# Performance work log

Measured on AMD Instinct MI355X. Metric: run time of the kernel, lower is better.

## Reference

```python
import jax, jax.numpy as jnp
import numpy as np

B, N, K = 8, 1024, 9
T = B * N
EPS_BN = 1e-5


def _knn_idx(x, k):
    # x: [n, d] -> [n, k] indices of k nearest neighbours (self included, dist 0)
    x = jax.lax.stop_gradient(x)
    sq = jnp.sum(x * x, axis=1)
    d = sq[:, None] + sq[None, :] - 2.0 * (x @ x.T)
    return jax.lax.top_k(-d, k)[1]


def _mlp_bn(x, params):
    # PyG MLP with plain_last=True: linear->BN->ReLU for all but last layer, last is linear.
    n = len(params)
    for i, (W, b, g, be) in enumerate(params):
        x = x @ W + b
        if i < n - 1:
            mu = jnp.mean(x, axis=0)
            var = jnp.var(x, axis=0)  # biased, as torch BN (training stats)
            x = g * (x - mu) * jax.lax.rsqrt(var + EPS_BN) + be
            x = jax.nn.relu(x)
    return x


def _edge_conv(x, idx, params):
    # DynamicEdgeConv: message = MLP([x_i, x_j - x_i]), aggr='mean' over k neighbours
    n, k = idx.shape
    xj = x[idx]                                   # [n,k,c] gather
    xi = jnp.broadcast_to(x[:, None, :], xj.shape)
    e = jnp.concatenate([xi, xj - xi], axis=-1).reshape(n * k, -1)
    h = _mlp_bn(e, params)                        # [n*k, c_out]
    return h.reshape(n, k, -1).mean(axis=1)       # mean aggregation


def _dgcnn(x, c1, c3, head, lin2_W, lin2_b):
    # conv1: kNN within each graph (batch-aware)
    xb = x.reshape(B, N, -1)
    idx = jax.vmap(lambda g: _knn_idx(g, K))(xb)                 # [B,N,K] local
    idx = (idx + (jnp.arange(B) * N)[:, None, None]).reshape(T, K)
    x1 = _edge_conv(x, idx, c1)                                  # [T,128]
    # head MLP (norm=None, dropout inactive in eval)
    h = x1
    for i, (W, b) in enumerate(head):
        h = h @ W + b
        if i < len(head) - 1:
            h = jax.nn.relu(h)
    out = (h - jnp.mean(h)) / (jnp.std(h, ddof=1) + 1e-5)        # torch.std unbiased
    out = jax.nn.sigmoid(out)                                    # [T,1] gate
    xl = out * x
    xs = (1.0 - out) * x
    # conv3 called without batch -> global kNN over all T nodes
    xl = _edge_conv(xl, _knn_idx(xl, K), c3)                     # [T,16]
    xs = _edge_conv(xs, _knn_idx(xs, K), c3)
    xl = xl.reshape(B, N, -1).max(axis=1)                        # global_max_pool
    xs = xs.reshape(B, N, -1).max(axis=1)
    mass = jnp.concatenate([xl, xs], axis=1) @ lin2_W + lin2_b   # [B,1]
    return mass.flatten()


_PARAM_SHAPES = {
    'c1_W1': (8, 128), 'c1_b1': (128,), 'c1_g1': (128,), 'c1_be1': (128,),
    'c1_W2': (128, 128), 'c1_b2': (128,), 'c1_g2': (128,), 'c1_be2': (128,),
    'c1_W3': (128, 128), 'c1_b3': (128,),
    'c3_W1': (8, 64), 'c3_b1': (64,), 'c3_g1': (64,), 'c3_be1': (64,),
    'c3_W2': (64, 64), 'c3_b2': (64,), 'c3_g2': (64,), 'c3_be2': (64,),
    'c3_W3': (64, 16), 'c3_b3': (16,),
    'h_W1': (128, 64), 'h_b1': (64,),
    'h_W2': (64, 32), 'h_b2': (32,),
    'h_W3': (32, 1), 'h_b3': (1,),
    'lin2_W': (32, 1), 'lin2_b': (1,),
}


def setup_inputs() -> dict:
    key = jax.random.key(0)
    ks = jax.random.split(key, len(_PARAM_SHAPES) + 1)
    inp = {'x': jax.random.normal(ks[0], (T, 4), dtype=jnp.float32)}
    for i, (name, shp) in enumerate(_PARAM_SHAPES.items()):
        v = jax.random.normal(ks[i + 1], shp, dtype=jnp.float32) * 0.1
        if '_g' in name:
            v = v + 1.0
        inp[name] = v
    return inp


def reference(x, c1_W1, c1_b1, c1_g1, c1_be1, c1_W2, c1_b2, c1_g2, c1_be2,
              c1_W3, c1_b3, c3_W1, c3_b1, c3_g1, c3_be1, c3_W2, c3_b2, c3_g2,
              c3_be2, c3_W3, c3_b3, h_W1, h_b1, h_W2, h_b2, h_W3, h_b3,
              lin2_W, lin2_b):
    c1 = [(c1_W1, c1_b1, c1_g1, c1_be1), (c1_W2, c1_b2, c1_g2, c1_be2),
          (c1_W3, c1_b3, None, None)]
    c3 = [(c3_W1, c3_b1, c3_g1, c3_be1), (c3_W2, c3_b2, c3_g2, c3_be2),
          (c3_W3, c3_b3, None, None)]
    head = [(h_W1, h_b1), (h_W2, h_b2), (h_W3, h_b3)]
    return _dgcnn(x, c1, c3, head, lin2_W, lin2_b)
```

## Files before the change

### kernel.cpp

```cpp
#include <hip/hip_runtime.h>
#include <math.h>

#define TN 8192
#define KNN 9
#define NPG 1024
#define TK (TN*KNN)
#define CPCL 12
#define NCHG 32
#define CPCG 16

__device__ __forceinline__ float sqnorm(float4 v){
  return fmaf(v.x,v.x,fmaf(v.y,v.y,fmaf(v.z,v.z,v.w*v.w)));
}
__device__ __forceinline__ float pairdist(float4 a, float sqa, float4 b, float sqb){
  float dot = fmaf(a.x,b.x,fmaf(a.y,b.y,fmaf(a.z,b.z,a.w*b.w)));
  return sqa + sqb - 2.0f*dot;
}
__device__ __forceinline__ void chain9(float (&bd)[9], float d){
  float t=d;
  #pragma unroll
  for(int p=0;p<9;p++){
    float lo=fminf(bd[p],t);
    t=fmaxf(bd[p],t);
    bd[p]=lo;
// ... 394 lines not shown

__global__ void k_bn2q(const double* __restrict__ Md, const float* __restrict__ W2,
      const float* __restrict__ g, const float* __restrict__ be,
      float* __restrict__ scale, float* __restrict__ shift){
  __shared__ double redq[128], redt[128];
  __shared__ float sw[128];
  int c = blockIdx.x, t = threadIdx.x;
  sw[t] = W2[t*128+c];
  __syncthreads();
  double zb = Md[16384+t]/(double)TK;
  double inner=0;
  for(int j=0;j<128;j++) inner += Md[t*128+j]*(double)sw[j];
  redq[t] = (double)sw[t]*(inner/(double)TK);
  redt[t] = (double)sw[t]*zb;
  __syncthreads();
  for(int s=64;s>0;s>>=1){
    if(t<s){ redq[t]+=redq[t+s]; redt[t]+=redt[t+s]; }
    __syncthreads();
  }
  if(t==0){
    double var = redq[0] - redt[0]*redt[0];
    if(var<0) var=0;
    double sc = (double)g[c]/sqrt(var+1e-5);
    scale[c]=(float)sc;
    shift[c]=(float)((double)be[c] - redt[0]*sc);
  }
}

__global__ __launch_bounds__(256) void k_midagg(const float4* __restrict__ x,
      const int* __restrict__ idx, const float* __restrict__ W1,
      const float* __restrict__ sc1, const float* __restrict__ sh1,
      const float* __restrict__ W2, const float* __restrict__ sc2,
      const float* __restrict__ sh2, float* __restrict__ Zb){
  __shared__ float sa[72][9];
  __shared__ float sW1[8*128];
  __shared__ float sZ[72*132];
  const int tid = threadIdx.x;
  const int node0 = blockIdx.x*8;
  if(tid<256) ((float4*)sW1)[tid] = ((const float4*)W1)[tid];
  if(tid<72){
    int e = blockIdx.x*72 + tid;
    int i = e/KNN; int j = idx[e];
    float4 xi = x[i], xj = x[j];
    sa[tid][0]=xi.x; sa[tid][1]=xi.y; sa[tid][2]=xi.z; sa[tid][3]=xi.w;
    sa[tid][4]=xj.x-xi.x; sa[tid][5]=xj.y-xi.y; sa[tid][6]=xj.z-xi.z; sa[tid][7]=xj.w-xi.w;
  }
  __syncthreads();
  for(int f=tid; f<2304; f+=256){
    int e = f>>5, c4 = f&31;
    float4 scv = ((const float4*)sc1)[c4];
    float4 shv = ((const float4*)sh1)[c4];
    float4 y = make_float4(0.f,0.f,0.f,0.f);
    #pragma unroll
    for(int k=0;k<8;k++){
      float a = sa[e][k];
      float4 wv = *(const float4*)(sW1 + k*128 + c4*4);
      y.x=fmaf(a,wv.x,y.x); y.y=fmaf(a,wv.y,y.y);
      y.z=fmaf(a,wv.z,y.z); y.w=fmaf(a,wv.w,y.w);
    }
    float4 z;
    z.x = fmaxf(fmaf(scv.x,y.x,shv.x),0.f);
    z.y = fmaxf(fmaf(scv.y,y.y,shv.y),0.f);
    z.z = fmaxf(fmaf(scv.z,y.z,shv.z),0.f);
    z.w = fmaxf(fmaf(scv.w,y.w,shv.w),0.f);
    *(float4*)(sZ + e*132 + c4*4) = z;
  }
  __syncthreads();
  const int tc = tid & 31, tr = tid >> 5;
  float acc[9][4];
  #pragma unroll
  for(int s=0;s<9;s++)
    #pragma unroll
    for(int e=0;e<4;e++) acc[s][e]=0.f;
  #pragma unroll 2
  for(int k4=0;k4<32;k4++){
    float4 av[9];
    #pragma unroll
    for(int s=0;s<9;s++) av[s] = *(const float4*)(sZ + (tr*9+s)*132 + k4*4);
    #pragma unroll
    for(int kk=0;kk<4;kk++){
      float4 bv = *(const float4*)(W2 + (size_t)(k4*4+kk)*128 + tc*4);
      #pragma unroll
      for(int s=0;s<9;s++){
        float a = (kk==0)?av[s].x:(kk==1)?av[s].y:(kk==2)?av[s].z:av[s].w;
        acc[s][0]=fmaf(a,bv.x,acc[s][0]);
        acc[s][1]=fmaf(a,bv.y,acc[s][1]);
        acc[s][2]=fmaf(a,bv.z,acc[s][2]);
        acc[s][3]=fmaf(a,bv.w,acc[s][3]);
      }
    }
  }
  float4 scv = ((const float4*)sc2)[tc];
  float4 shv = ((const float4*)sh2)[tc];
  float4 sum = make_float4(0.f,0.f,0.f,0.f);
  #pragma unroll
  for(int s=0;s<9;s++){
    sum.x += fmaxf(fmaf(scv.x,acc[s][0],shv.x),0.f);
    sum.y += fmaxf(fmaf(scv.y,acc[s][1],shv.y),0.f);
    sum.z += fmaxf(fmaf(scv.z,acc[s][2],shv.z),0.f);
    sum.w += fmaxf(fmaf(scv.w,acc[s][3],shv.w),0.f);
  }
  sum.x*=(1.f/9.f); sum.y*=(1.f/9.f); sum.z*=(1.f/9.f); sum.w*=(1.f/9.f);
  *(float4*)(Zb + (size_t)(node0+tr)*128 + tc*4) = sum;
}

__global__ __launch_bounds__(256) void k_gemm128(const float* __restrict__ A,
      const float* __restrict__ W, const float* __restrict__ bias,
      float* __restrict__ out){
  __shared__ float sZ[64*132];
  const int tid = threadIdx.x;
  const int row0 = blockIdx.x*64;
  for(int e=tid; e<64*32; e+=256){
    int r = e>>5, c4 = e&31;
    ((float4*)(sZ + r*132))[c4] = ((const float4*)(A + (size_t)(row0+r)*128))[c4];
  }
  __syncthreads();
  const int tc = tid & 31, tr = tid >> 5;
  float acc[8][4];
  #pragma unroll
  for(int rr=0;rr<8;rr++)
    #pragma unroll
    for(int e=0;e<4;e++) acc[rr][e]=0.f;
  #pragma unroll 4
  for(int k4=0;k4<32;k4++){
    float4 av[8];
    #pragma unroll
    for(int rr=0;rr<8;rr++) av[rr] = *(const float4*)(sZ + (tr+rr*8)*132 + k4*4);
    #pragma unroll
    for(int kk=0;kk<4;kk++){
      float4 bv = *(const float4*)(W + (size_t)(k4*4+kk)*128 + tc*4);
      #pragma unroll
      for(int rr=0;rr<8;rr++){
        float a = (kk==0)?av[rr].x:(kk==1)?av[rr].y:(kk==2)?av[rr].z:av[rr].w;
        acc[rr][0]=fmaf(a,bv.x,acc[rr][0]);
        acc[rr][1]=fmaf(a,bv.y,acc[rr][1]);
        acc[rr][2]=fmaf(a,bv.z,acc[rr][2]);
        acc[rr][3]=fmaf(a,bv.w,acc[rr][3]);
      }
    }
  }
  float4 breg = *(const float4*)(bias + tc*4);
  #pragma unroll
  for(int rr=0;rr<8;rr++){
    int r = row0 + tr + rr*8;
    float4 vals;
    vals.x = acc[rr][0]+breg.x;
    vals.y = acc[rr][1]+breg.y;
    vals.z = acc[rr][2]+breg.z;
    vals.w = acc[rr][3]+breg.w;
    *(float4*)(out + (size_t)r*128 + tc*4) = vals;
  }
}

__global__ __launch_bounds__(256) void k_l1d(const float4* __restrict__ xa,
        const float4* __restrict__ xb, const int* __restrict__ ia,
        const int* __restrict__ ib, const float* __restrict__ W,
        const float* __restrict__ bias, float* __restrict__ Ybase,
        float* __restrict__ pstat){
  constexpr int NOUT = 64;
  __shared__ float sA[64][9];
  __shared__ float sW[8*NOUT];
  __shared__ float ssum[NOUT], ssq2[NOUT];
  const int by = blockIdx.y;
  const float4* x = by ? xb : xa;
  const int* idx = by ? ib : ia;
  float* Y = Ybase + (size_t)by*TK*NOUT;
  const int tid = threadIdx.x;
  const int row0 = blockIdx.x*64;
  if(tid < 64){
    int r = row0 + tid;
    int i = r/KNN;
    int j = idx[r];
    float4 xi = x[i], xj = x[j];
    sA[tid][0]=xi.x; sA[tid][1]=xi.y; sA[tid][2]=xi.z; sA[tid][3]=xi.w;
    sA[tid][4]=xj.x-xi.x; sA[tid][5]=xj.y-xi.y; sA[tid][6]=xj.z-xi.z; sA[tid][7]=xj.w-xi.w;
  }
  for(int e=tid; e<8*NOUT/4; e+=256) ((float4*)sW)[e] = ((const float4*)W)[e];
  if(tid < NOUT){ ssum[tid]=0.f; ssq2[tid]=0.f; }
  __syncthreads();
  const int tc = tid & 15, tr = tid >> 4;
  float acc[4][4];
  #pragma unroll
  for(int rr=0;rr<4;rr++)
    #pragma unroll
    for(int cc=0;cc<4;cc++) acc[rr][cc]=0.f;
  #pragma unroll
  for(int k=0;k<8;k++){
    float a[4];
    #pragma unroll
    for(int rr=0;rr<4;rr++) a[rr]=sA[tr*4+rr][k];
    #pragma unroll
    for(int cc=0;cc<4;cc++){
      float bv = sW[k*NOUT + tc*4 + cc];
      #pragma unroll
      for(int rr=0;rr<4;rr++) acc[rr][cc]=fmaf(a[rr],bv,acc[rr][cc]);
    }
  }
  float breg[4];
  #pragma unroll
  for(int cc=0;cc<4;cc++) breg[cc]=bias[tc*4+cc];
  float ls[4], lq[4];
  #pragma unroll
  for(int cc=0;cc<4;cc++){ls[cc]=0.f;lq[cc]=0.f;}
  #pragma unroll
  for(int rr=0;rr<4;rr++){
    int r = row0 + tr*4 + rr;
    float vals[4];
    #pragma unroll
    for(int u=0;u<4;u++){
      float val = acc[rr][u] + breg[u];
      vals[u]=val; ls[u]+=val; lq[u]+=val*val;
    }
    *(float4*)(Y + (size_t)r*NOUT + tc*4) = make_float4(vals[0],vals[1],vals[2],vals[3]);
  }
  #pragma unroll
  for(int cc=0;cc<4;cc++){
    atomicAdd(&ssum[tc*4+cc], ls[cc]);
    atomicAdd(&ssq2[tc*4+cc], lq[cc]);
  }
  __syncthreads();
  if(tid < NOUT){
    size_t pb = ((size_t)by*1152 + blockIdx.x)*2*NOUT;
    pstat[pb + tid] = ssum[tid];
    pstat[pb + NOUT + tid] = ssq2[tid];
  }
}

__global__ __launch_bounds__(256) void k_psum(const float* __restrict__ pstat,
      double* __restrict__ pp, int nblk, int twoC){
  size_t base = (size_t)blockIdx.y*nblk*twoC;
  int per = (nblk+7)/8;
  int b0 = blockIdx.x*per;
  int b1 = b0+per; if(b1>nblk) b1=nblk;
  for(int e=threadIdx.x; e<twoC; e+=256){
    double s=0;
    for(int b=b0;b<b1;b++) s += (double)pstat[base + (size_t)b*twoC + e];
    pp[((size_t)blockIdx.y*8 + blockIdx.x)*twoC + e] = s;
  }
}

__global__ void k_finalized(const double* __restrict__ pp,
     const float* __restrict__ g, const float* __restrict__ be,
     float* __restrict__ scale, float* __restrict__ shift, double M){
  int prob = threadIdx.x >> 6, c = threadIdx.x & 63;
  double S=0,Q=0;
  for(int b=0;b<8;b++){
    S+=pp[((size_t)prob*8+b)*128 + c];
    Q+=pp[((size_t)prob*8+b)*128 + 64 + c];
  }
  double mu = S/M;
  double var = Q/M - mu*mu;
  if(var < 0) var = 0;
  double sc = (double)g[c] / sqrt(var + 1e-5);
  scale[prob*64+c] = (float)sc;
  shift[prob*64+c] = (float)((double)be[c] - mu*sc);
}

__global__ __launch_bounds__(512,4) void k_mid64d(float* __restrict__ Ybase,
        const float* __restrict__ W, const float* __restrict__ bias,
        const float* __restrict__ scale2, const float* __restrict__ shift2,
        float* __restrict__ pstat){
  constexpr int C = 64;
  constexpr int CPAD = 68;
  __shared__ float sZ[128*CPAD];
  __shared__ float sW[64*C];
  __shared__ float ssum[C], ssq2[C];
  const int by = blockIdx.y;
  float* Y = Ybase + (size_t)by*TK*C;
  const float* scale = scale2 + by*C;
  const float* shift = shift2 + by*C;
  const int tid = threadIdx.x;
  const int row0 = blockIdx.x*128;
  for(int e=tid; e<128*16; e+=512){
    int r = e>>4, c4 = e&15;
    float4 v = ((const float4*)(Y + (size_t)(row0+r)*C))[c4];
    float4 sc = ((const float4*)scale)[c4];
    float4 sh = ((const float4*)shift)[c4];
    v.x = fmaxf(fmaf(sc.x,v.x,sh.x), 0.f);
    v.y = fmaxf(fmaf(sc.y,v.y,sh.y), 0.f);
    v.z = fmaxf(fmaf(sc.z,v.z,sh.z), 0.f);
    v.w = fmaxf(fmaf(sc.w,v.w,sh.w), 0.f);
    ((float4*)(sZ + r*CPAD))[c4] = v;
  }
  for(int e=tid; e<64*C/4; e+=512) ((float4*)sW)[e] = ((const float4*)W)[e];
  if(tid < C){ ssum[tid]=0.f; ssq2[tid]=0.f; }
  __syncthreads();
  const int tc = tid & 15, tr = tid >> 4;
  float acc[4][4];
  #pragma unroll
  for(int rr=0;rr<4;rr++)
    #pragma unroll
    for(int e=0;e<4;e++) acc[rr][e]=0.f;
  #pragma unroll 4
  for(int k4=0;k4<16;k4++){
    float4 av[4];
    #pragma unroll
    for(int rr=0;rr<4;rr++) av[rr] = *(const float4*)(sZ + (tr+rr*32)*CPAD + k4*4);
    #pragma unroll
    for(int kk=0;kk<4;kk++){
      float4 bv = *(const float4*)(sW + (k4*4+kk)*C + tc*4);
      #pragma unroll
      for(int rr=0;rr<4;rr++){
        float a = (kk==0)?av[rr].x:(kk==1)?av[rr].y:(kk==2)?av[rr].z:av[rr].w;
        acc[rr][0]=fmaf(a,bv.x,acc[rr][0]);
        acc[rr][1]=fmaf(a,bv.y,acc[rr][1]);
        acc[rr][2]=fmaf(a,bv.z,acc[rr][2]);
        acc[rr][3]=fmaf(a,bv.w,acc[rr][3]);
      }
    }
  }
  float4 breg = *(const float4*)(bias + tc*4);
  float ls[4]={0,0,0,0}, lq[4]={0,0,0,0};
  #pragma unroll
  for(int rr=0;rr<4;rr++){
    int r = row0 + tr + rr*32;
    float4 vals;
    vals.x = acc[rr][0]+breg.x;
    vals.y = acc[rr][1]+breg.y;
    vals.z = acc[rr][2]+breg.z;
    vals.w = acc[rr][3]+breg.w;
    ls[0]+=vals.x; lq[0]+=vals.x*vals.x;
    ls[1]+=vals.y; lq[1]+=vals.y*vals.y;
    ls[2]+=vals.z; lq[2]+=vals.z*vals.z;
    ls[3]+=vals.w; lq[3]+=vals.w*vals.w;
    *(float4*)(Y + (size_t)r*C + tc*4) = vals;
  }
  #pragma unroll
  for(int e=0;e<4;e++){
    atomicAdd(&ssum[tc*4+e], ls[e]);
    atomicAdd(&ssq2[tc*4+e], lq[e]);
  }
  __syncthreads();
  if(tid < C){
    size_t pb = ((size_t)by*576 + blockIdx.x)*2*C;
    pstat[pb + tid] = ssum[tid];
    pstat[pb + C + tid] = ssq2[tid];
  }
}

__global__ __launch_bounds__(256) void k_agg_gemmd(const float* __restrict__ Ybase,
      const float* __restrict__ scale2, const float* __restrict__ shift2,
      const float* __restrict__ W, const float* __restrict__ bias,
      float* __restrict__ outl, float* __restrict__ outs){
  constexpr int KIN=64, NOUT=16;
  constexpr int CPAD = KIN+4;
  __shared__ float sZ[64*CPAD];
  __shared__ float sW[KIN*NOUT];
  const int by = blockIdx.y;
  const float* Y = Ybase + (size_t)by*TK*KIN;
  const float* scale = scale2 + by*KIN;
  const float* shift = shift2 + by*KIN;
  float* out = by ? outs : outl;
  const int tid = threadIdx.x;
  const int node0 = blockIdx.x*64;
  for(int e=tid; e<64*KIN/4; e+=256){
    int r = e/(KIN/4), c4 = e%(KIN/4);
    float4 sc = ((const float4*)scale)[c4];
    float4 sh = ((const float4*)shift)[c4];
    const float4* src = (const float4*)(Y + (size_t)(node0+r)*KNN*KIN) + c4;
    float4 s = make_float4(0.f,0.f,0.f,0.f);
    #pragma unroll
    for(int j=0;j<KNN;j++){
      float4 v = src[(size_t)j*(KIN/4)];
      s.x += fmaxf(fmaf(sc.x,v.x,sh.x),0.f);
      s.y += fmaxf(fmaf(sc.y,v.y,sh.y),0.f);
      s.z += fmaxf(fmaf(sc.z,v.z,sh.z),0.f);
      s.w += fmaxf(fmaf(sc.w,v.w,sh.w),0.f);
    }
    s.x*=(1.f/9.f); s.y*=(1.f/9.f); s.z*=(1.f/9.f); s.w*=(1.f/9.f);
    ((float4*)(sZ + r*CPAD))[c4] = s;
  }
  for(int e=tid; e<KIN*NOUT/4; e+=256) ((float4*)sW)[e] = ((const float4*)W)[e];
  __syncthreads();
  const int tc = tid & 15, tr = tid >> 4;
  float acc[4] = {0.f,0.f,0.f,0.f};
  for(int k4=0;k4<KIN/4;k4++){
    float4 av[4];
    #pragma unroll
    for(int rr=0;rr<4;rr++) av[rr] = *(const float4*)(sZ + (tr+rr*16)*CPAD + k4*4);
    #pragma unroll
    for(int kk=0;kk<4;kk++){
      float bv = sW[(k4*4+kk)*NOUT + tc];
      #pragma unroll
      for(int rr=0;rr<4;rr++){
        float a = (kk==0)?av[rr].x:(kk==1)?av[rr].y:(kk==2)?av[rr].z:av[rr].w;
        acc[rr]=fmaf(a,bv,acc[rr]);
      }
    }
  }
  #pragma unroll
  for(int rr=0;rr<4;rr++){
    int r = node0 + tr + rr*16;
    out[(size_t)r*NOUT + tc] = acc[rr] + bias[tc];
  }
}

__global__ __launch_bounds__(256) void k_head(const float* __restrict__ x1,
    const float* __restrict__ W1, const float* __restrict__ b1,
    const float* __restrict__ W2, const float* __restrict__ b2,
    const float* __restrict__ W3, const float* __restrict__ b3,
    float* __restrict__ h, float* __restrict__ pstat){
  __shared__ float sA[32*132];
  __shared__ float sW1[128*64];
  __shared__ float o1[32*68];
  __shared__ float sW2[64*32];
  __shared__ float o2[32*33];
  __shared__ float sb1[64], sb2[32], sW3v[32];
  __shared__ float rs[32], rq[32];
  const int tid = threadIdx.x;
  const int row0 = blockIdx.x*32;
  for(int e=tid; e<32*32; e+=256){
    int r = e>>5, c4 = e&31;
    ((float4*)(sA + r*132))[c4] = ((const float4*)(x1 + (size_t)(row0+r)*128))[c4];
  }
  for(int e=tid; e<128*64/4; e+=256) ((float4*)sW1)[e] = ((const float4*)W1)[e];
  for(int e=tid; e<64*32/4; e+=256)  ((float4*)sW2)[e] = ((const float4*)W2)[e];
  if(tid < 64) sb1[tid]=b1[tid];
  if(tid < 32){ sb2[tid]=b2[tid]; sW3v[tid]=W3[tid]; }
  __syncthreads();
  const int tc = tid & 15, tr = tid >> 4;
  float a1[2][4];
  #pragma unroll
  for(int rr=0;rr<2;rr++)
    #pragma unroll
    for(int e=0;e<4;e++) a1[rr][e]=0.f;
  for(int k4=0;k4<32;k4++){
    float4 av0 = *(const float4*)(sA + (tr*2  )*132 + k4*4);
    float4 av1 = *(const float4*)(sA + (tr*2+1)*132 + k4*4);
    #pragma unroll
    for(int kk=0;kk<4;kk++){
      float4 bv = *(const float4*)(sW1 + (k4*4+kk)*64 + tc*4);
      float p0 = (kk==0)?av0.x:(kk==1)?av0.y:(kk==2)?av0.z:av0.w;
      float p1 = (kk==0)?av1.x:(kk==1)?av1.y:(kk==2)?av1.z:av1.w;
      a1[0][0]=fmaf(p0,bv.x,a1[0][0]); a1[0][1]=fmaf(p0,bv.y,a1[0][1]);
      a1[0][2]=fmaf(p0,bv.z,a1[0][2]); a1[0][3]=fmaf(p0,bv.w,a1[0][3]);
      a1[1][0]=fmaf(p1,bv.x,a1[1][0]); a1[1][1]=fmaf(p1,bv.y,a1[1][1]);
      a1[1][2]=fmaf(p1,bv.z,a1[1][2]); a1[1][3]=fmaf(p1,bv.w,a1[1][3]);
    }
  }
  #pragma unroll
  for(int rr=0;rr<2;rr++)
    #pragma unroll
    for(int e=0;e<4;e++)
      o1[(tr*2+rr)*68 + tc*4+e] = fmaxf(a1[rr][e]+sb1[tc*4+e], 0.f);
  __syncthreads();
  float a2[2][2] = {{0.f,0.f},{0.f,0.f}};
  for(int k=0;k<64;k++){
    float w0 = sW2[k*32 + tc*2], w1 = sW2[k*32 + tc*2+1];
    float v0 = o1[(tr*2  )*68 + k];
    float v1 = o1[(tr*2+1)*68 + k];
    a2[0][0]=fmaf(v0,w0,a2[0][0]); a2[0][1]=fmaf(v0,w1,a2[0][1]);
    a2[1][0]=fmaf(v1,w0,a2[1][0]); a2[1][1]=fmaf(v1,w1,a2[1][1]);
  }
  #pragma unroll
  for(int rr=0;rr<2;rr++)
    #pragma unroll
    for(int cc=0;cc<2;cc++)
      o2[(tr*2+rr)*33 + tc*2+cc] = fmaxf(a2[rr][cc]+sb2[tc*2+cc], 0.f);
  __syncthreads();
  if(tid < 32){
    float hv = b3[0];
    #pragma unroll
    for(int k=0;k<32;k++) hv = fmaf(o2[tid*33+k], sW3v[k], hv);
    h[row0+tid]=hv;
    rs[tid]=hv; rq[tid]=hv*hv;
  }
  __syncthreads();
  if(tid==0){
    float S=0.f, Q=0.f;
    #pragma unroll
    for(int i=0;i<32;i++){ S+=rs[i]; Q+=rq[i]; }
    pstat[blockIdx.x*2]=S; pstat[blockIdx.x*2+1]=Q;
  }
}

__global__ __launch_bounds__(256) void k_fin_h(const float* __restrict__ pstat,
      float* __restrict__ hpar){
  __shared__ double sS[256], sQ[256];
  int t = threadIdx.x;
  sS[t] = (double)pstat[2*t]; sQ[t] = (double)pstat[2*t+1];
  __syncthreads();
  for(int s=128;s>0;s>>=1){
    if(t<s){ sS[t]+=sS[t+s]; sQ[t]+=sQ[t+s]; }
    __syncthreads();
  }
  if(t==0){
    double mu = sS[0]/8192.0;
    double var = (sQ[0] - 8192.0*mu*mu)/8191.0;
    double sd = (var > 0) ? sqrt(var) : 0.0;
    hpar[0]=(float)mu;
    hpar[1]=(float)(1.0/(sd + 1e-5));
  }
}

__global__ __launch_bounds__(256) void k_gate(const float* __restrict__ h,
      const float* __restrict__ hpar, const float4* __restrict__ x,
      float4* __restrict__ xl, float4* __restrict__ xs){
  int i = blockIdx.x*256 + threadIdx.x;
  float z = (h[i]-hpar[0])*hpar[1];
  float o = 1.0f/(1.0f+expf(-z));
  float om = 1.0f - o;
  float4 v = x[i];
  xl[i] = make_float4(o*v.x, o*v.y, o*v.z, o*v.w);
  xs[i] = make_float4(om*v.x, om*v.y, om*v.z, om*v.w);
}

__global__ __launch_bounds__(256) void k_final(const float* __restrict__ xlf,
      const float* __restrict__ xsf, const float* __restrict__ W,
      const float* __restrict__ b, float* __restrict__ out){
  __shared__ float red[32][8];
  int g = blockIdx.x;
  int c = threadIdx.x & 31;
  int chunk = threadIdx.x >> 5;
  const float* src = (c < 16) ? xlf : xsf;
  int ch = (c < 16) ? c : c-16;
  float m = -1e30f;
  for(int n=chunk*128; n<chunk*128+128; n++)
    m = fmaxf(m, src[((size_t)g*1024+n)*16 + ch]);
  red[c][chunk]=m;
  __syncthreads();
  if(threadIdx.x < 32){
    float mm = red[threadIdx.x][0];
    #pragma unroll
    for(int p=1;p<8;p++) mm = fmaxf(mm, red[threadIdx.x][p]);
    red[threadIdx.x][0]=mm;
  }
  __syncthreads();
  if(threadIdx.x == 0){
    float acc = b[0];
    for(int cc=0;cc<32;cc++) acc = fmaf(red[cc][0], W[cc], acc);
    out[g]=acc;
  }
}

extern "C" void kernel_launch(void* const* d_in, const int* in_sizes, int n_in,
                              void* d_out, int out_size, void* d_ws, size_t ws_size,
                              hipStream_t stream){
  const float* x    =(const float*)d_in[0];
  const float* c1W1 =(const float*)d_in[1];
  const float* c1g1 =(const float*)d_in[3];
  const float* c1be1=(const float*)d_in[4];
  const float* c1W2 =(const float*)d_in[5];
  const float* c1g2 =(const float*)d_in[7];
  const float* c1be2=(const float*)d_in[8];
  const float* c1W3 =(const float*)d_in[9];
  const float* c1b3 =(const float*)d_in[10];
  const float* c3W1 =(const float*)d_in[11];
  const float* c3b1 =(const float*)d_in[12];
  const float* c3g1 =(const float*)d_in[13];
  const float* c3be1=(const float*)d_in[14];
  const float* c3W2 =(const float*)d_in[15];
  const float* c3b2 =(const float*)d_in[16];
  const float* c3g2 =(const float*)d_in[17];
  const float* c3be2=(const float*)d_in[18];
  const float* c3W3 =(const float*)d_in[19];
  const float* c3b3 =(const float*)d_in[20];
  const float* hW1  =(const float*)d_in[21];
  const float* hb1  =(const float*)d_in[22];
  const float* hW2  =(const float*)d_in[23];
  const float* hb2  =(const float*)d_in[24];
  const float* hW3  =(const float*)d_in[25];
  const float* hb3  =(const float*)d_in[26];
  const float* l2W  =(const float*)d_in[27];
  const float* l2b  =(const float*)d_in[28];
  (void)in_sizes; (void)n_in; (void)out_size; (void)ws_size;

  char* wsb=(char*)d_ws;
  size_t off=0;
  auto alloc=[&](size_t bytes)->char*{
    char* p = wsb + off;
    off = (off + bytes + 255) & ~(size_t)255;
    return p;
  };
  float* Y    =(float*)alloc((size_t)TK*128*4);
  float* x1   =(float*)alloc((size_t)TN*128*4);
  float* Zb   =(float*)alloc((size_t)TN*128*4);
  int*   idx1 =(int*)  alloc((size_t)TK*4);
  int*   idxl =(int*)  alloc((size_t)TK*4);
  int*   idxs =(int*)  alloc((size_t)TK*4);
  float* pd   =(float*)alloc((size_t)2*TN*72*4);
  float* h    =(float*)alloc((size_t)TN*4);
  float* xl   =(float*)alloc((size_t)TN*16);
  float* xs   =(float*)alloc((size_t)TN*16);
  float* xlf  =(float*)alloc((size_t)TN*16*4);
  float* xsf  =(float*)alloc((size_t)TN*16*4);
  float* pstat=(float*)alloc((size_t)2304*128*4);
  double* pp  =(double*)alloc((size_t)16*256*8);
  double* Md  =(double*)alloc((size_t)16512*8);
  float* mp44 =(float*)alloc((size_t)288*44*4);
  float* tl   =(float*)alloc((size_t)TN*4);
  float* tg   =(float*)alloc((size_t)2*TN*4);
  unsigned char* cnt8l=(unsigned char*)alloc((size_t)TN*8);
  unsigned char* cnt8g=(unsigned char*)alloc((size_t)2*TN*NCHG);
  float* bnp  =(float*)alloc(1024*4);
  float* hpar =(float*)alloc(64);

  float* sc1=bnp,      *sh1=bnp+128, *sc2=bnp+256, *sh2=bnp+384;
  float* scA=bnp+512,  *shA=bnp+640, *scB=bnp+768, *shB=bnp+896;
  unsigned short* listl=(unsigned short*)Y;
  unsigned short* listg=(unsigned short*)Y;
  float* mpartM = Y;

  k_part_local  <<<256,256,0,stream>>>((const float4*)x, pd);
  k_thresh_local<<<32, 256,0,stream>>>(pd, tl);
  k_collect_local<<<256,256,0,stream>>>((const float4*)x, tl, cnt8l, listl);
  k_refine_local<<<TN/32,256,0,stream>>>((const float4*)x, cnt8l, listl, idx1);
  k_mom8<<<288,256,0,stream>>>((const float4*)x, idx1, mp44);
  k_bn1q<<<1,128,0,stream>>>(mp44, c1W1, c1g1, c1be1, sc1, sh1);
  k_syrk128<<<288,256,0,stream>>>((const float4*)x, idx1, c1W1, sc1, sh1, mpartM);
  k_redM<<<65,256,0,stream>>>(mpartM, Md);
  k_bn2q<<<128,128,0,stream>>>(Md, c1W2, c1g2, c1be2, sc2, sh2);
  k_midagg<<<1024,256,0,stream>>>((const float4*)x, idx1, c1W1, sc1, sh1, c1W2, sc2, sh2, Zb);
  k_gemm128<<<TN/64,256,0,stream>>>(Zb, c1W3, c1b3, x1);
  k_head<<<TN/32,256,0,stream>>>(x1,hW1,hb1,hW2,hb2,hW3,hb3,h,pstat);
  k_fin_h<<<1,256,0,stream>>>(pstat,hpar);
  k_gate<<<32,256,0,stream>>>(h,hpar,(const float4*)x,(float4*)xl,(float4*)xs);
  k_part_sub   <<<dim3(256,2),256,0,stream>>>((const float4*)xl,(const float4*)xs,pd);
  k_thresh_sub <<<64,256,0,stream>>>(pd,tg);
  k_collect_glob<<<dim3(512,2),256,0,stream>>>((const float4*)xl,(const float4*)xs,tg,cnt8g,listg);
  k_refine_glob<<<2*TN/32,256,0,stream>>>((const float4*)xl,(const float4*)xs,cnt8g,listg,idxl,idxs);
  k_l1d<<<dim3(1152,2),256,0,stream>>>((const float4*)xl,(const float4*)xs,idxl,idxs,c3W1,c3b1,Y,pstat);
  k_psum<<<dim3(8,2),256,0,stream>>>(pstat, pp, 1152, 128);
  k_finalized<<<1,128,0,stream>>>(pp,c3g1,c3be1,scA,shA,(double)TK);
  k_mid64d<<<dim3(576,2),512,0,stream>>>(Y, c3W2, c3b2, scA, shA, pstat);
  k_psum<<<dim3(8,2),256,0,stream>>>(pstat, pp, 576, 128);
  k_finalized<<<1,128,0,stream>>>(pp,c3g2,c3be2,scB,shB,(double)TK);
  k_agg_gemmd<<<dim3(TN/64,2),256,0,stream>>>(Y, scB, shB, c3W3, c3b3, xlf, xsf);
  k_final<<<8,256,0,stream>>>(xlf,xsf,l2W,l2b,(float*)d_out);
}
```

Baseline: 497.9 us.

## Compute conv3 BatchNorm stats via input moments and Gram matrix, fuse mean-aggregation

The conv3 edge-MLP no longer writes the [TK,64] layer-1 and layer-2 activations to global memory. BN1 statistics now come from first and second moments of the 8-wide edge features projected through W1. BN2 statistics come from a 64x64 Gram matrix of the post-BN1 activations, accumulated per block and reduced in double precision. A fused kernel then recomputes layer1, layer2, BN, ReLU and the mean over the 9 neighbours in shared memory, applying W3 after aggregation. This trades heavy global memory traffic for recomputation and a syrk pass, and relies on the biases cancelling under BN.

```diff
diff --git a/kernel.cpp b/kernel.cpp
--- a/kernel.cpp
+++ b/kernel.cpp
@@ -570,235 +570,289 @@
   }
 }
 
-__global__ __launch_bounds__(256) void k_l1d(const float4* __restrict__ xa,
-        const float4* __restrict__ xb, const int* __restrict__ ia,
-        const int* __restrict__ ib, const float* __restrict__ W,
-        const float* __restrict__ bias, float* __restrict__ Ybase,
-        float* __restrict__ pstat){
-  constexpr int NOUT = 64;
-  __shared__ float sA[64][9];
-  __shared__ float sW[8*NOUT];
-  __shared__ float ssum[NOUT], ssq2[NOUT];
-  const int by = blockIdx.y;
-  const float4* x = by ? xb : xa;
-  const int* idx = by ? ib : ia;
-  float* Y = Ybase + (size_t)by*TK*NOUT;
+__global__ __launch_bounds__(256) void k_mom8d(const float4* __restrict__ xa,
+      const float4* __restrict__ xb, const int* __restrict__ ia,
+      const int* __restrict__ ib, float* __restrict__ mpart){
+  __shared__ float sa[256][9];
+  const int prob = blockIdx.y;
+  const float4* x = prob ? xb : xa;
+  const int* idx = prob ? ib : ia;
+  int t = threadIdx.x;
+  int e = blockIdx.x*256 + t;
+  int i = e/KNN; int j = idx[e];
+  float4 xi = x[i], xj = x[j];
+  sa[t][0]=xi.x; sa[t][1]=xi.y; sa[t][2]=xi.z; sa[t][3]=xi.w;
+  sa[t][4]=xj.x-xi.x; sa[t][5]=xj.y-xi.y; sa[t][6]=xj.z-xi.z; sa[t][7]=xj.w-xi.w;
+  __syncthreads();
+  if(t < 44){
+    float s=0.f;
+    if(t<8){
+      for(int e2=0;e2<256;e2++) s += sa[e2][t];
+    } else {
+      int f=t-8, p=0, q=0, acc=0;
+      for(p=0;p<8;p++){ int cnt=8-p; if(f<acc+cnt){ q=p+(f-acc); break;} acc+=cnt; }
+      for(int e2=0;e2<256;e2++) s += sa[e2][p]*sa[e2][q];
+    }
+    mpart[((size_t)prob*288 + blockIdx.x)*44 + t]=s;
+  }
+}
+
+__global__ void k_bn1qd(const float* __restrict__ mpart, const float* __restrict__ W1,
+      const float* __restrict__ g, const float* __restrict__ be,
+      float* __restrict__ scale, float* __restrict__ shift){
+  __shared__ double mom[2][44];
+  int t = threadIdx.x;
+  if(t<88){
+    int pr=t/44, m=t%44;
+    double s=0; for(int b=0;b<288;b++) s+=(double)mpart[((size_t)pr*288+b)*44+m];
+    mom[pr][m]=s;
+  }
+  __syncthreads();
+  int prob = t>>6, c = t&63;
+  double m[8], w[8];
+  #pragma unroll
+  for(int p=0;p<8;p++){ m[p]=mom[prob][p]/(double)TK; w[p]=(double)W1[p*64+c]; }
+  double q=0.0; int f=8;
+  for(int p=0;p<8;p++)
+    for(int qq=p;qq<8;qq++){
+      double cov = mom[prob][f]/(double)TK - m[p]*m[qq];
+      q += (p==qq?1.0:2.0)*w[p]*w[qq]*cov;
+      f++;
+    }
+  if(q<0) q=0;
+  double sc = (double)g[c]/sqrt(q+1e-5);
+  double mu=0; for(int p=0;p<8;p++) mu += m[p]*w[p];
+  scale[prob*64+c]=(float)sc;
+  shift[prob*64+c]=(float)((double)be[c] - mu*sc);
+}
+
+__global__ __launch_bounds__(256) void k_syrk64d(const float4* __restrict__ xa,
+      const float4* __restrict__ xb, const int* __restrict__ ia,
+      const int* __restrict__ ib, const float* __restrict__ W1,
+      const float* __restrict__ sc0, const float* __restrict__ sh0,
+      float* __restrict__ mpartM){
+  __shared__ float sa[64][9];
+  __shared__ float sW1[8*64];
+  __shared__ float sZ[64*68];
+  __shared__ float ssum[64];
+  const int prob = blockIdx.y;
+  const float4* x = prob ? xb : xa;
+  const int* idx = prob ? ib : ia;
+  const float* sc1 = sc0 + prob*64;
+  const float* sh1 = sh0 + prob*64;
+  const int tid = threadIdx.x;
+  if(tid<128) ((float4*)sW1)[tid] = ((const float4*)W1)[tid];
+  if(tid<64) ssum[tid]=0.f;
+  const int zc4 = tid & 15, ze0 = tid >> 4;
+  const int i0 = (tid>>4)*4, j0 = (tid&15)*4;
+  float acc[4][4];
+  #pragma unroll
+  for(int a=0;a<4;a++)
+    #pragma unroll
+    for(int b=0;b<4;b++) acc[a][b]=0.f;
+  float ls[4]={0,0,0,0};
+  float4 scv = ((const float4*)sc1)[zc4];
+  float4 shv = ((const float4*)sh1)[zc4];
+  for(int pass=0;pass<4;pass++){
+    __syncthreads();
+    if(tid<64){
+      int e = blockIdx.x*256 + pass*64 + tid;
+      int i = e/KNN; int j = idx[e];
+      float4 xi = x[i], xj = x[j];
+      sa[tid][0]=xi.x; sa[tid][1]=xi.y; sa[tid][2]=xi.z; sa[tid][3]=xi.w;
+      sa[tid][4]=xj.x-xi.x; sa[tid][5]=xj.y-xi.y; sa[tid][6]=xj.z-xi.z; sa[tid][7]=xj.w-xi.w;
+    }
+    __syncthreads();
+    for(int e=ze0; e<64; e+=16){
+      float4 y = make_float4(0.f,0.f,0.f,0.f);
+      #pragma unroll
+      for(int k=0;k<8;k++){
+        float a = sa[e][k];
+        float4 wv = *(const float4*)(sW1 + k*64 + zc4*4);
+        y.x=fmaf(a,wv.x,y.x); y.y=fmaf(a,wv.y,y.y);
+        y.z=fmaf(a,wv.z,y.z); y.w=fmaf(a,wv.w,y.w);
+      }
+      float4 z;
+      z.x = fmaxf(fmaf(scv.x,y.x,shv.x),0.f);
+      z.y = fmaxf(fmaf(scv.y,y.y,shv.y),0.f);
+      z.z = fmaxf(fmaf(scv.z,y.z,shv.z),0.f);
+      z.w = fmaxf(fmaf(scv.w,y.w,shv.w),0.f);
+      *(float4*)(sZ + e*68 + zc4*4) = z;
+      ls[0]+=z.x; ls[1]+=z.y; ls[2]+=z.z; ls[3]+=z.w;
+    }
+    __syncthreads();
+    #pragma unroll 4
+    for(int e=0;e<64;e++){
+      const float* rz = sZ + e*68;
+      float4 zi4 = *(const float4*)(rz + i0);
+      float4 zj4 = *(const float4*)(rz + j0);
+      float zi[4]={zi4.x,zi4.y,zi4.z,zi4.w};
+      float zj[4]={zj4.x,zj4.y,zj4.z,zj4.w};
+      #pragma unroll
+      for(int a=0;a<4;a++)
+        #pragma unroll
+        for(int b=0;b<4;b++) acc[a][b]=fmaf(zi[a],zj[b],acc[a][b]);
+    }
+  }
+  #pragma unroll
+  for(int c=0;c<4;c++) atomicAdd(&ssum[zc4*4+c], ls[c]);
+  float* mp = mpartM + ((size_t)prob*288 + blockIdx.x)*4160;
+  #pragma unroll
+  for(int a=0;a<4;a++)
+    *(float4*)(mp + (i0+a)*64 + j0) = make_float4(acc[a][0],acc[a][1],acc[a][2],acc[a][3]);
+  __syncthreads();
+  if(tid<64) mp[4096+tid] = ssum[tid];
+}
+
+__global__ __launch_bounds__(256) void k_redMd(const float* __restrict__ mpartM,
+      double* __restrict__ Md){
+  int ch = blockIdx.x*256 + threadIdx.x;
+  if(ch >= 8320) return;
+  int prob = ch / 4160, c = ch % 4160;
+  double s=0;
+  for(int b=0;b<288;b++) s += (double)mpartM[((size_t)prob*288+b)*4160 + c];
+  Md[(size_t)prob*4160 + c]=s;
+}
+
+__global__ void k_bn2qd(const double* __restrict__ Md, const float* __restrict__ W2,
+      const float* __restrict__ g, const float* __restrict__ be,
+      float* __restrict__ scale, float* __restrict__ shift){
+  __shared__ double redq[64], redt[64];
+  __shared__ float sw[64];
+  int c = blockIdx.x, prob = blockIdx.y, t = threadIdx.x;
+  const double* md = Md + (size_t)prob*4160;
+  sw[t] = W2[t*64+c];
+  __syncthreads();
+  double zb = md[4096+t]/(double)TK;
+  double inner=0;
+  for(int j=0;j<64;j++) inner += md[t*64+j]*(double)sw[j];
+  redq[t] = (double)sw[t]*(inner/(double)TK);
+  redt[t] = (double)sw[t]*zb;
+  __syncthreads();
+  for(int s=32;s>0;s>>=1){
+    if(t<s){ redq[t]+=redq[t+s]; redt[t]+=redt[t+s]; }
+    __syncthreads();
+  }
+  if(t==0){
+    double var = redq[0] - redt[0]*redt[0];
+    if(var<0) var=0;
+    double sc = (double)g[c]/sqrt(var+1e-5);
+    scale[prob*64+c]=(float)sc;
+    shift[prob*64+c]=(float)((double)be[c] - redt[0]*sc);
+  }
+}
+
+__global__ __launch_bounds__(256) void k_midagg64d(const float4* __restrict__ xa,
+      const float4* __restrict__ xb, const int* __restrict__ ia,
+      const int* __restrict__ ib, const float* __restrict__ W1,
+      const float* __restrict__ sc0, const float* __restrict__ sh0,
+      const float* __restrict__ W2, const float* __restrict__ sc20,
+      const float* __restrict__ sh20, float* __restrict__ Zb64){
+  __shared__ float sa[144][9];
+  __shared__ float sW1[8*64];
+  __shared__ float sZ[144*68];
+  const int prob = blockIdx.y;
+  const float4* x = prob ? xb : xa;
+  const int* idx = prob ? ib : ia;
+  const float* sc1 = sc0 + prob*64;
+  const float* sh1 = sh0 + prob*64;
+  const float* sc2 = sc20 + prob*64;
+  const float* sh2 = sh20 + prob*64;
+  const int tid = threadIdx.x;
+  const int node0 = blockIdx.x*16;
+  if(tid<128) ((float4*)sW1)[tid] = ((const float4*)W1)[tid];
+  if(tid<144){
+    int e = blockIdx.x*144 + tid;
+    int i = e/KNN; int j = idx[e];
+    float4 xi = x[i], xj = x[j];
+    sa[tid][0]=xi.x; sa[tid][1]=xi.y; sa[tid][2]=xi.z; sa[tid][3]=xi.w;
+    sa[tid][4]=xj.x-xi.x; sa[tid][5]=xj.y-xi.y; sa[tid][6]=xj.z-xi.z; sa[tid][7]=xj.w-xi.w;
+  }
+  __syncthreads();
+  for(int f=tid; f<144*16; f+=256){
+    int e = f>>4, c4 = f&15;
+    float4 scv = ((const float4*)sc1)[c4];
+    float4 shv = ((const float4*)sh1)[c4];
+    float4 y = make_float4(0.f,0.f,0.f,0.f);
+    #pragma unroll
+    for(int k=0;k<8;k++){
+      float a = sa[e][k];
+      float4 wv = *(const float4*)(sW1 + k*64 + c4*4);
+      y.x=fmaf(a,wv.x,y.x); y.y=fmaf(a,wv.y,y.y);
+      y.z=fmaf(a,wv.z,y.z); y.w=fmaf(a,wv.w,y.w);
+    }
+    float4 z;
+    z.x = fmaxf(fmaf(scv.x,y.x,shv.x),0.f);
+    z.y = fmaxf(fmaf(scv.y,y.y,shv.y),0.f);
+    z.z = fmaxf(fmaf(scv.z,y.z,shv.z),0.f);
+    z.w = fmaxf(fmaf(scv.w,y.w,shv.w),0.f);
+    *(float4*)(sZ + e*68 + c4*4) = z;
+  }
+  __syncthreads();
+  const int cg = tid & 15, nd = tid >> 4;
+  float acc[9][4];
+  #pragma unroll
+  for(int s=0;s<9;s++)
+    #pragma unroll
+    for(int e=0;e<4;e++) acc[s][e]=0.f;
+  #pragma unroll 2
+  for(int k4=0;k4<16;k4++){
+    float4 av[9];
+    #pragma unroll
+    for(int s=0;s<9;s++) av[s] = *(const float4*)(sZ + (nd*9+s)*68 + k4*4);
+    #pragma unroll
+    for(int kk=0;kk<4;kk++){
+      float4 bv = *(const float4*)(W2 + (size_t)(k4*4+kk)*64 + cg*4);
+      #pragma unroll
+      for(int s=0;s<9;s++){
+        float a = (kk==0)?av[s].x:(kk==1)?av[s].y:(kk==2)?av[s].z:av[s].w;
+        acc[s][0]=fmaf(a,bv.x,acc[s][0]);
+        acc[s][1]=fmaf(a,bv.y,acc[s][1]);
+        acc[s][2]=fmaf(a,bv.z,acc[s][2]);
+        acc[s][3]=fmaf(a,bv.w,acc[s][3]);
+      }
+    }
+  }
+  float4 scv = ((const float4*)sc2)[cg];
+  float4 shv = ((const float4*)sh2)[cg];
+  float4 sum = make_float4(0.f,0.f,0.f,0.f);
+  #pragma unroll
+  for(int s=0;s<9;s++){
+    sum.x += fmaxf(fmaf(scv.x,acc[s][0],shv.x),0.f);
+    sum.y += fmaxf(fmaf(scv.y,acc[s][1],shv.y),0.f);
+    sum.z += fmaxf(fmaf(scv.z,acc[s][2],shv.z),0.f);
+    sum.w += fmaxf(fmaf(scv.w,acc[s][3],shv.w),0.f);
+  }
+  sum.x*=(1.f/9.f); sum.y*=(1.f/9.f); sum.z*=(1.f/9.f); sum.w*=(1.f/9.f);
+  *(float4*)(Zb64 + ((size_t)prob*TN + node0+nd)*64 + cg*4) = sum;
+}
+
+__global__ __launch_bounds__(256) void k_gemm16d(const float* __restrict__ Zb64,
+      const float* __restrict__ W, const float* __restrict__ bias,
+      float* __restrict__ outl, float* __restrict__ outs){
+  __shared__ float sZ[64*68];
+  __shared__ float sW[64*16];
+  const int prob = blockIdx.y;
+  const float* A = Zb64 + (size_t)prob*TN*64;
+  float* out = prob ? outs : outl;
   const int tid = threadIdx.x;
   const int row0 = blockIdx.x*64;
-  if(tid < 64){
-    int r = row0 + tid;
-    int i = r/KNN;
-    int j = idx[r];
-    float4 xi = x[i], xj = x[j];
-    sA[tid][0]=xi.x; sA[tid][1]=xi.y; sA[tid][2]=xi.z; sA[tid][3]=xi.w;
-    sA[tid][4]=xj.x-xi.x; sA[tid][5]=xj.y-xi.y; sA[tid][6]=xj.z-xi.z; sA[tid][7]=xj.w-xi.w;
-  }
-  for(int e=tid; e<8*NOUT/4; e+=256) ((float4*)sW)[e] = ((const float4*)W)[e];
-  if(tid < NOUT){ ssum[tid]=0.f; ssq2[tid]=0.f; }
+  for(int e=tid; e<64*16; e+=256){
+    int r = e>>4, c4 = e&15;
+    ((float4*)(sZ + r*68))[c4] = ((const float4*)(A + (size_t)(row0+r)*64))[c4];
+  }
+  ((float4*)sW)[tid] = ((const float4*)W)[tid];
   __syncthreads();
   const int tc = tid & 15, tr = tid >> 4;
-  float acc[4][4];
-  #pragma unroll
-  for(int rr=0;rr<4;rr++)
-    #pragma unroll
-    for(int cc=0;cc<4;cc++) acc[rr][cc]=0.f;
-  #pragma unroll
-  for(int k=0;k<8;k++){
-    float a[4];
-    #pragma unroll
-    for(int rr=0;rr<4;rr++) a[rr]=sA[tr*4+rr][k];
-    #pragma unroll
-    for(int cc=0;cc<4;cc++){
-      float bv = sW[k*NOUT + tc*4 + cc];
-      #pragma unroll
-      for(int rr=0;rr<4;rr++) acc[rr][cc]=fmaf(a[rr],bv,acc[rr][cc]);
-    }
-  }
-  float breg[4];
-  #pragma unroll
-  for(int cc=0;cc<4;cc++) breg[cc]=bias[tc*4+cc];
-  float ls[4], lq[4];
-  #pragma unroll
-  for(int cc=0;cc<4;cc++){ls[cc]=0.f;lq[cc]=0.f;}
-  #pragma unroll
-  for(int rr=0;rr<4;rr++){
-    int r = row0 + tr*4 + rr;
-    float vals[4];
-    #pragma unroll
-    for(int u=0;u<4;u++){
-      float val = acc[rr][u] + breg[u];
-      vals[u]=val; ls[u]+=val; lq[u]+=val*val;
-    }
-    *(float4*)(Y + (size_t)r*NOUT + tc*4) = make_float4(vals[0],vals[1],vals[2],vals[3]);
-  }
-  #pragma unroll
-  for(int cc=0;cc<4;cc++){
-    atomicAdd(&ssum[tc*4+cc], ls[cc]);
-    atomicAdd(&ssq2[tc*4+cc], lq[cc]);
-  }
-  __syncthreads();
-  if(tid < NOUT){
-    size_t pb = ((size_t)by*1152 + blockIdx.x)*2*NOUT;
-    pstat[pb + tid] = ssum[tid];
-    pstat[pb + NOUT + tid] = ssq2[tid];
-  }
-}
-
-__global__ __launch_bounds__(256) void k_psum(const float* __restrict__ pstat,
-      double* __restrict__ pp, int nblk, int twoC){
-  size_t base = (size_t)blockIdx.y*nblk*twoC;
-  int per = (nblk+7)/8;
-  int b0 = blockIdx.x*per;
-  int b1 = b0+per; if(b1>nblk) b1=nblk;
-  for(int e=threadIdx.x; e<twoC; e+=256){
-    double s=0;
-    for(int b=b0;b<b1;b++) s += (double)pstat[base + (size_t)b*twoC + e];
-    pp[((size_t)blockIdx.y*8 + blockIdx.x)*twoC + e] = s;
-  }
-}
-
-__global__ void k_finalized(const double* __restrict__ pp,
-     const float* __restrict__ g, const float* __restrict__ be,
-     float* __restrict__ scale, float* __restrict__ shift, double M){
-  int prob = threadIdx.x >> 6, c = threadIdx.x & 63;
-  double S=0,Q=0;
-  for(int b=0;b<8;b++){
-    S+=pp[((size_t)prob*8+b)*128 + c];
-    Q+=pp[((size_t)prob*8+b)*128 + 64 + c];
-  }
-  double mu = S/M;
-  double var = Q/M - mu*mu;
-  if(var < 0) var = 0;
-  double sc = (double)g[c] / sqrt(var + 1e-5);
-  scale[prob*64+c] = (float)sc;
-  shift[prob*64+c] = (float)((double)be[c] - mu*sc);
-}
-
-__global__ __launch_bounds__(512,4) void k_mid64d(float* __restrict__ Ybase,
-        const float* __restrict__ W, const float* __restrict__ bias,
-        const float* __restrict__ scale2, const float* __restrict__ shift2,
-        float* __restrict__ pstat){
-  constexpr int C = 64;
-  constexpr int CPAD = 68;
-  __shared__ float sZ[128*CPAD];
-  __shared__ float sW[64*C];
-  __shared__ float ssum[C], ssq2[C];
-  const int by = blockIdx.y;
-  float* Y = Ybase + (size_t)by*TK*C;
-  const float* scale = scale2 + by*C;
-  const float* shift = shift2 + by*C;
-  const int tid = threadIdx.x;
-  const int row0 = blockIdx.x*128;
-  for(int e=tid; e<128*16; e+=512){
-    int r = e>>4, c4 = e&15;
-    float4 v = ((const float4*)(Y + (size_t)(row0+r)*C))[c4];
-    float4 sc = ((const float4*)scale)[c4];
-    float4 sh = ((const float4*)shift)[c4];
-    v.x = fmaxf(fmaf(sc.x,v.x,sh.x), 0.f);
-    v.y = fmaxf(fmaf(sc.y,v.y,sh.y), 0.f);
-    v.z = fmaxf(fmaf(sc.z,v.z,sh.z), 0.f);
-    v.w = fmaxf(fmaf(sc.w,v.w,sh.w), 0.f);
-    ((float4*)(sZ + r*CPAD))[c4] = v;
-  }
-  for(int e=tid; e<64*C/4; e+=512) ((float4*)sW)[e] = ((const float4*)W)[e];
-  if(tid < C){ ssum[tid]=0.f; ssq2[tid]=0.f; }
-  __syncthreads();
-  const int tc = tid & 15, tr = tid >> 4;
-  float acc[4][4];
-  #pragma unroll
-  for(int rr=0;rr<4;rr++)
-    #pragma unroll
-    for(int e=0;e<4;e++) acc[rr][e]=0.f;
+  float acc[4] = {0.f,0.f,0.f,0.f};
   #pragma unroll 4
   for(int k4=0;k4<16;k4++){
     float4 av[4];
     #pragma unroll
-    for(int rr=0;rr<4;rr++) av[rr] = *(const float4*)(sZ + (tr+rr*32)*CPAD + k4*4);
+    for(int rr=0;rr<4;rr++) av[rr] = *(const float4*)(sZ + (tr+rr*16)*68 + k4*4);
     #pragma unroll
     for(int kk=0;kk<4;kk++){
-      float4 bv = *(const float4*)(sW + (k4*4+kk)*C + tc*4);
-      #pragma unroll
-      for(int rr=0;rr<4;rr++){
-        float a = (kk==0)?av[rr].x:(kk==1)?av[rr].y:(kk==2)?av[rr].z:av[rr].w;
-        acc[rr][0]=fmaf(a,bv.x,acc[rr][0]);
-        acc[rr][1]=fmaf(a,bv.y,acc[rr][1]);
-        acc[rr][2]=fmaf(a,bv.z,acc[rr][2]);
-        acc[rr][3]=fmaf(a,bv.w,acc[rr][3]);
-      }
-    }
-  }
-  float4 breg = *(const float4*)(bias + tc*4);
-  float ls[4]={0,0,0,0}, lq[4]={0,0,0,0};
-  #pragma unroll
-  for(int rr=0;rr<4;rr++){
-    int r = row0 + tr + rr*32;
-    float4 vals;
-    vals.x = acc[rr][0]+breg.x;
-    vals.y = acc[rr][1]+breg.y;
-    vals.z = acc[rr][2]+breg.z;
-    vals.w = acc[rr][3]+breg.w;
-    ls[0]+=vals.x; lq[0]+=vals.x*vals.x;
-    ls[1]+=vals.y; lq[1]+=vals.y*vals.y;
-    ls[2]+=vals.z; lq[2]+=vals.z*vals.z;
-    ls[3]+=vals.w; lq[3]+=vals.w*vals.w;
-    *(float4*)(Y + (size_t)r*C + tc*4) = vals;
-  }
-  #pragma unroll
-  for(int e=0;e<4;e++){
-    atomicAdd(&ssum[tc*4+e], ls[e]);
-    atomicAdd(&ssq2[tc*4+e], lq[e]);
-  }
-  __syncthreads();
-  if(tid < C){
-    size_t pb = ((size_t)by*576 + blockIdx.x)*2*C;
-    pstat[pb + tid] = ssum[tid];
-    pstat[pb + C + tid] = ssq2[tid];
-  }
-}
-
-__global__ __launch_bounds__(256) void k_agg_gemmd(const float* __restrict__ Ybase,
-      const float* __restrict__ scale2, const float* __restrict__ shift2,
-      const float* __restrict__ W, const float* __restrict__ bias,
-      float* __restrict__ outl, float* __restrict__ outs){
-  constexpr int KIN=64, NOUT=16;
-  constexpr int CPAD = KIN+4;
-  __shared__ float sZ[64*CPAD];
-  __shared__ float sW[KIN*NOUT];
-  const int by = blockIdx.y;
-  const float* Y = Ybase + (size_t)by*TK*KIN;
-  const float* scale = scale2 + by*KIN;
-  const float* shift = shift2 + by*KIN;
-  float* out = by ? outs : outl;
-  const int tid = threadIdx.x;
-  const int node0 = blockIdx.x*64;
-  for(int e=tid; e<64*KIN/4; e+=256){
-    int r = e/(KIN/4), c4 = e%(KIN/4);
-    float4 sc = ((const float4*)scale)[c4];
-    float4 sh = ((const float4*)shift)[c4];
-    const float4* src = (const float4*)(Y + (size_t)(node0+r)*KNN*KIN) + c4;
-    float4 s = make_float4(0.f,0.f,0.f,0.f);
-    #pragma unroll
-    for(int j=0;j<KNN;j++){
-      float4 v = src[(size_t)j*(KIN/4)];
-      s.x += fmaxf(fmaf(sc.x,v.x,sh.x),0.f);
-      s.y += fmaxf(fmaf(sc.y,v.y,sh.y),0.f);
-      s.z += fmaxf(fmaf(sc.z,v.z,sh.z),0.f);
-      s.w += fmaxf(fmaf(sc.w,v.w,sh.w),0.f);
-    }
-    s.x*=(1.f/9.f); s.y*=(1.f/9.f); s.z*=(1.f/9.f); s.w*=(1.f/9.f);
-    ((float4*)(sZ + r*CPAD))[c4] = s;
-  }
-  for(int e=tid; e<KIN*NOUT/4; e+=256) ((float4*)sW)[e] = ((const float4*)W)[e];
-  __syncthreads();
-  const int tc = tid & 15, tr = tid >> 4;
-  float acc[4] = {0.f,0.f,0.f,0.f};
-  for(int k4=0;k4<KIN/4;k4++){
-    float4 av[4];
-    #pragma unroll
-    for(int rr=0;rr<4;rr++) av[rr] = *(const float4*)(sZ + (tr+rr*16)*CPAD + k4*4);
-    #pragma unroll
-    for(int kk=0;kk<4;kk++){
-      float bv = sW[(k4*4+kk)*NOUT + tc];
+      float bv = sW[(k4*4+kk)*16 + tc];
       #pragma unroll
       for(int rr=0;rr<4;rr++){
         float a = (kk==0)?av[rr].x:(kk==1)?av[rr].y:(kk==2)?av[rr].z:av[rr].w;
@@ -808,8 +862,8 @@
   }
   #pragma unroll
   for(int rr=0;rr<4;rr++){
-    int r = node0 + tr + rr*16;
-    out[(size_t)r*NOUT + tc] = acc[rr] + bias[tc];
+    int r = row0 + tr + rr*16;
+    out[(size_t)r*16 + tc] = acc[rr] + bias[tc];
   }
 }
 
@@ -964,11 +1018,9 @@
   const float* c1W3 =(const float*)d_in[9];
   const float* c1b3 =(const float*)d_in[10];
   const float* c3W1 =(const float*)d_in[11];
-  const float* c3b1 =(const float*)d_in[12];
   const float* c3g1 =(const float*)d_in[13];
   const float* c3be1=(const float*)d_in[14];
   const float* c3W2 =(const float*)d_in[15];
-  const float* c3b2 =(const float*)d_in[16];
   const float* c3g2 =(const float*)d_in[17];
   const float* c3be2=(const float*)d_in[18];
   const float* c3W3 =(const float*)d_in[19];
@@ -1002,10 +1054,11 @@
   float* xs   =(float*)alloc((size_t)TN*16);
   float* xlf  =(float*)alloc((size_t)TN*16*4);
   float* xsf  =(float*)alloc((size_t)TN*16*4);
-  float* pstat=(float*)alloc((size_t)2304*128*4);
-  double* pp  =(double*)alloc((size_t)16*256*8);
+  float* pstat=(float*)alloc((size_t)512*4);
   double* Md  =(double*)alloc((size_t)16512*8);
+  double* Mdd =(double*)alloc((size_t)8320*8);
   float* mp44 =(float*)alloc((size_t)288*44*4);
+  float* mp44d=(float*)alloc((size_t)2*288*44*4);
   float* tl   =(float*)alloc((size_t)TN*4);
   float* tg   =(float*)alloc((size_t)2*TN*4);
   unsigned char* cnt8l=(unsigned char*)alloc((size_t)TN*8);
@@ -1018,6 +1071,7 @@
   unsigned short* listl=(unsigned short*)Y;
   unsigned short* listg=(unsigned short*)Y;
   float* mpartM = Y;
+  float* mpartMd = Y;
 
   k_part_local  <<<256,256,0,stream>>>((const float4*)x, pd);
   k_thresh_local<<<32, 256,0,stream>>>(pd, tl);
@@ -1037,12 +1091,13 @@
   k_thresh_sub <<<64,256,0,stream>>>(pd,tg);
   k_collect_glob<<<dim3(512,2),256,0,stream>>>((const float4*)xl,(const float4*)xs,tg,cnt8g,listg);
   k_refine_glob<<<2*TN/32,256,0,stream>>>((const float4*)xl,(const float4*)xs,cnt8g,listg,idxl,idxs);
-  k_l1d<<<dim3(1152,2),256,0,stream>>>((const float4*)xl,(const float4*)xs,idxl,idxs,c3W1,c3b1,Y,pstat);
-  k_psum<<<dim3(8,2),256,0,stream>>>(pstat, pp, 1152, 128);
-  k_finalized<<<1,128,0,stream>>>(pp,c3g1,c3be1,scA,shA,(double)TK);
-  k_mid64d<<<dim3(576,2),512,0,stream>>>(Y, c3W2, c3b2, scA, shA, pstat);
-  k_psum<<<dim3(8,2),256,0,stream>>>(pstat, pp, 576, 128);
-  k_finalized<<<1,128,0,stream>>>(pp,c3g2,c3be2,scB,shB,(double)TK);
-  k_agg_gemmd<<<dim3(TN/64,2),256,0,stream>>>(Y, scB, shB, c3W3, c3b3, xlf, xsf);
+  k_mom8d<<<dim3(288,2),256,0,stream>>>((const float4*)xl,(const float4*)xs,idxl,idxs,mp44d);
+  k_bn1qd<<<1,128,0,stream>>>(mp44d, c3W1, c3g1, c3be1, scA, shA);
+  k_syrk64d<<<dim3(288,2),256,0,stream>>>((const float4*)xl,(const float4*)xs,idxl,idxs,c3W1,scA,shA,mpartMd);
+  k_redMd<<<33,256,0,stream>>>(mpartMd, Mdd);
+  k_bn2qd<<<dim3(64,2),64,0,stream>>>(Mdd, c3W2, c3g2, c3be2, scB, shB);
+  k_midagg64d<<<dim3(512,2),256,0,stream>>>((const float4*)xl,(const float4*)xs,idxl,idxs,
+      c3W1, scA, shA, c3W2, scB, shB, Zb);
+  k_gemm16d<<<dim3(TN/64,2),256,0,stream>>>(Zb, c3W3, c3b3, xlf, xsf);
   k_final<<<8,256,0,stream>>>(xlf,xsf,l2W,l2b,(float*)d_out);
 }
```

New measurement: 450.7 us. 1.1x faster.
